# Optimization experiments

Measured on AMD Instinct MI355X. Metric: run time of the kernel, lower is better.

The kernel has to match this reference:

```python
import jax, jax.numpy as jnp
import numpy as np

N, M, P = 128, 16, 256   # speakers, utterances/speaker, projection dim
W, B = 10.0, -5.0        # GE2E scale/bias (abs(w)*s + b)
EPS_NORM = 1e-12
EPS_LOG = 1e-9


def setup_inputs() -> dict:
    key = jax.random.key(0)
    e = jax.random.normal(key, (N * M, P), dtype=jnp.float32)
    return {"e": e}


def _l2norm(x):
    return x / jnp.sqrt(jnp.sum(x * x, axis=-1, keepdims=True) + EPS_NORM)


def _similarity(e):
    # i_eq_j: [N*M, N], row k has 1 in column k//M
    eye = jnp.repeat(jnp.eye(N, dtype=e.dtype), M, axis=0)
    i = eye[:, :, None]                               # [N*M, N, 1]
    spk = e.reshape(N, M, P)
    cent_sum = jnp.sum(spk, axis=1)                   # [N, P] full centroid sums
    # leave-one-out subtraction only where i==j: [N*M, N, P]
    centroids = cent_sum[None, :, :] - i * e[:, None, :]
    # scale: /(m-1) for own speaker (leave-one-out), /m otherwise
    centroids = (i / (M - 1) + (1.0 - i) / M) * centroids
    e_n = _l2norm(e)                                  # [N*M, P]
    c_n = _l2norm(centroids)                          # [N*M, N, P]
    s = jnp.einsum('kp,knp->kn', e_n, c_n)            # [N*M, N]
    return s


def reference(e):
    eye = jnp.repeat(jnp.eye(N, dtype=e.dtype), M, axis=0)
    s = jnp.abs(W) * _similarity(e) + B               # [N*M, N]
    s_jij = jnp.sum(s * eye, axis=-1)                 # [N*M]
    softmax = jnp.log(jnp.sum(jnp.exp(s), axis=-1) + EPS_LOG)
    loss = jnp.mean(-s_jij + softmax)
    return (loss, s)
```

## Files before the change

kernel.cpp:

```cpp
#include <hip/hip_runtime.h>
#include <math.h>

#define N_CL 128
#define M_SPK 16
#define P_DIM 256
#define NM 2048
static constexpr float EPS_NORM = 1e-12f;
static constexpr float EPS_LOG  = 1e-9f;
static constexpr float W_ABS    = 10.0f;
static constexpr float B_OFF    = -5.0f;

#define WS_CENTT   0
#define WS_CSN     32768
#define WS_SCALE   32896
#define WS_ENORM2  33024
#define WS_RE      35072
#define WS_ROWLOSS 37120

__device__ __forceinline__ float waveReduceSum(float x) {
    #pragma unroll
    for (int off = 32; off > 0; off >>= 1)
        x += __shfl_xor(x, off, 64);
    return x;
}

__global__ __launch_bounds__(256)
void k1_stats(const float* __restrict__ e, float* __restrict__ ws) {
    const int n    = blockIdx.x;
    const int p    = threadIdx.x;
    const int wid  = p >> 6;
    const int lane = p & 63;

    float* centT     = ws + WS_CENTT;
    float* csn       = ws + WS_CSN;
    float* scale_oth = ws + WS_SCALE;
    float* enorm2    = ws + WS_ENORM2;
    float* re        = ws + WS_RE;

    __shared__ float part[M_SPK][4];
    __shared__ float cpart[4];

    float acc = 0.f;
    #pragma unroll
    for (int m = 0; m < M_SPK; ++m) {
        float v = e[(n * M_SPK + m) * P_DIM + p];
        acc += v;
        float sq = waveReduceSum(v * v);
        if (lane == 0) part[m][wid] = sq;
    }
    centT[p * N_CL + n] = acc;

    float c2 = waveReduceSum(acc * acc);
    if (lane == 0) cpart[wid] = c2;
    __syncthreads();

    if (p < M_SPK) {
        int row = n * M_SPK + p;
        float s2 = part[p][0] + part[p][1] + part[p][2] + part[p][3];
        enorm2[row] = s2;
        re[row] = 1.0f / sqrtf(s2 + EPS_NORM);
    }
    if (p == 0) {
        float t = cpart[0] + cpart[1] + cpart[2] + cpart[3];
        csn[n] = t;
        scale_oth[n] = 1.0f / sqrtf(t + (float)(M_SPK * M_SPK) * EPS_NORM);
    }
}

__global__ __launch_bounds__(128)
void k2_main(const float* __restrict__ e, const float* __restrict__ ws,
             float* __restrict__ d_out, float* __restrict__ rowloss) {
    const int k = blockIdx.x;
    const int t = threadIdx.x;

    const float* centT     = ws + WS_CENTT;
    const float* csn       = ws + WS_CSN;
    const float* scale_oth = ws + WS_SCALE;
    const float* enorm2    = ws + WS_ENORM2;
    const float* re        = ws + WS_RE;

    __shared__ float eL[P_DIM];
    __shared__ float wpart[2];
    __shared__ float sOwn;

    eL[t]       = e[k * P_DIM + t];
    eL[t + 128] = e[k * P_DIM + 128 + t];
    __syncthreads();

    float dot = 0.f;
    #pragma unroll 16
    for (int p = 0; p < P_DIM; ++p)
        dot = fmaf(eL[p], centT[p * N_CL + t], dot);

    const int nk = k >> 4;
    const float rek = re[k];
    float s;
    if (t == nk) {
        const float e2  = enorm2[k];
        const float num = (dot - e2) * (1.0f / (M_SPK - 1));
        const float h2  = (csn[nk] - 2.0f * dot + e2)
                          * (1.0f / ((M_SPK - 1) * (M_SPK - 1)));
        s = W_ABS * (num * rek / sqrtf(h2 + EPS_NORM)) + B_OFF;
        sOwn = s;
    } else {
        s = W_ABS * (dot * rek * scale_oth[t]) + B_OFF;
    }
    d_out[1 + k * N_CL + t] = s;

    float ex = expf(s);
    float wsum = waveReduceSum(ex);
    const int lane = t & 63;
    const int wid  = t >> 6;
    if (lane == 0) wpart[wid] = wsum;
    __syncthreads();
    if (t == 0) {
        float tot = wpart[0] + wpart[1];
        rowloss[k] = logf(tot + EPS_LOG) - sOwn;
    }
}

__global__ __launch_bounds__(256)
void k3_reduce(const float* __restrict__ rowloss, float* __restrict__ d_out) {
    __shared__ float wpart[4];
    const int t = threadIdx.x;
    float sum = 0.f;
    #pragma unroll
    for (int i = 0; i < NM / 256; ++i)
        sum += rowloss[i * 256 + t];
    sum = waveReduceSum(sum);
    if ((t & 63) == 0) wpart[t >> 6] = sum;
    __syncthreads();
    if (t == 0)
        d_out[0] = (wpart[0] + wpart[1] + wpart[2] + wpart[3]) * (1.0f / NM);
}

extern "C" void kernel_launch(void* const* d_in, const int* in_sizes, int n_in,
                              void* d_out, int out_size, void* d_ws, size_t ws_size,
                              hipStream_t stream) {
    const float* e = (const float*)d_in[0];
    float* out = (float*)d_out;
    float* ws  = (float*)d_ws;

    k1_stats<<<N_CL, 256, 0, stream>>>(e, ws);
    k2_main<<<NM, 128, 0, stream>>>(e, ws, out, ws + WS_ROWLOSS);
    k3_reduce<<<1, 256, 0, stream>>>(ws + WS_ROWLOSS, out);
}
```

Baseline: 23.99 us.

## Fuse similarity and loss reduction into one kernel with last-block atomic reduce

Removes the third reduction kernel by having the last finishing block of the main kernel sum per-block losses, detected through an atomic counter. Each block now handles 8 rows instead of one, so every centroid load is reused across 4 rows per wave. Row and centroid norms are recomputed inside the main kernel instead of being precomputed in a stats kernel, which slims the first kernel. This trades a launch and some redundant norm work for more register pressure and an atomic-ordering dependency.

```diff
diff --git a/kernel.cpp b/kernel.cpp
--- a/kernel.cpp
+++ b/kernel.cpp
@@ -5,17 +5,13 @@
 #define M_SPK 16
 #define P_DIM 256
 #define NM 2048
+#define NBLK 256
 static constexpr float EPS_NORM = 1e-12f;
 static constexpr float EPS_LOG  = 1e-9f;
-static constexpr float W_ABS    = 10.0f;
-static constexpr float B_OFF    = -5.0f;
 
-#define WS_CENTT   0
-#define WS_CSN     32768
-#define WS_SCALE   32896
-#define WS_ENORM2  33024
-#define WS_RE      35072
-#define WS_ROWLOSS 37120
+#define WS_CENTT     0
+#define WS_BLOCKLOSS 32768
+#define WS_CNT       33024
 
 __device__ __forceinline__ float waveReduceSum(float x) {
     #pragma unroll
@@ -25,113 +21,130 @@
 }
 
 __global__ __launch_bounds__(256)
-void k1_stats(const float* __restrict__ e, float* __restrict__ ws) {
-    const int n    = blockIdx.x;
-    const int p    = threadIdx.x;
-    const int wid  = p >> 6;
-    const int lane = p & 63;
-
-    float* centT     = ws + WS_CENTT;
-    float* csn       = ws + WS_CSN;
-    float* scale_oth = ws + WS_SCALE;
-    float* enorm2    = ws + WS_ENORM2;
-    float* re        = ws + WS_RE;
-
-    __shared__ float part[M_SPK][4];
-    __shared__ float cpart[4];
-
+void k1_cent(const float* __restrict__ e, float* __restrict__ ws,
+             unsigned* __restrict__ cnt) {
+    const int n = blockIdx.x;
+    const int p = threadIdx.x;
+    const float* base = e + (size_t)n * (M_SPK * P_DIM) + p;
     float acc = 0.f;
     #pragma unroll
-    for (int m = 0; m < M_SPK; ++m) {
-        float v = e[(n * M_SPK + m) * P_DIM + p];
-        acc += v;
-        float sq = waveReduceSum(v * v);
-        if (lane == 0) part[m][wid] = sq;
-    }
-    centT[p * N_CL + n] = acc;
-
-    float c2 = waveReduceSum(acc * acc);
-    if (lane == 0) cpart[wid] = c2;
-    __syncthreads();
-
-    if (p < M_SPK) {
-        int row = n * M_SPK + p;
-        float s2 = part[p][0] + part[p][1] + part[p][2] + part[p][3];
-        enorm2[row] = s2;
-        re[row] = 1.0f / sqrtf(s2 + EPS_NORM);
-    }
-    if (p == 0) {
-        float t = cpart[0] + cpart[1] + cpart[2] + cpart[3];
-        csn[n] = t;
-        scale_oth[n] = 1.0f / sqrtf(t + (float)(M_SPK * M_SPK) * EPS_NORM);
-    }
-}
-
-__global__ __launch_bounds__(128)
-void k2_main(const float* __restrict__ e, const float* __restrict__ ws,
-             float* __restrict__ d_out, float* __restrict__ rowloss) {
-    const int k = blockIdx.x;
-    const int t = threadIdx.x;
-
-    const float* centT     = ws + WS_CENTT;
-    const float* csn       = ws + WS_CSN;
-    const float* scale_oth = ws + WS_SCALE;
-    const float* enorm2    = ws + WS_ENORM2;
-    const float* re        = ws + WS_RE;
-
-    __shared__ float eL[P_DIM];
-    __shared__ float wpart[2];
-    __shared__ float sOwn;
-
-    eL[t]       = e[k * P_DIM + t];
-    eL[t + 128] = e[k * P_DIM + 128 + t];
-    __syncthreads();
-
-    float dot = 0.f;
-    #pragma unroll 16
-    for (int p = 0; p < P_DIM; ++p)
-        dot = fmaf(eL[p], centT[p * N_CL + t], dot);
-
-    const int nk = k >> 4;
-    const float rek = re[k];
-    float s;
-    if (t == nk) {
-        const float e2  = enorm2[k];
-        const float num = (dot - e2) * (1.0f / (M_SPK - 1));
-        const float h2  = (csn[nk] - 2.0f * dot + e2)
-                          * (1.0f / ((M_SPK - 1) * (M_SPK - 1)));
-        s = W_ABS * (num * rek / sqrtf(h2 + EPS_NORM)) + B_OFF;
-        sOwn = s;
-    } else {
-        s = W_ABS * (dot * rek * scale_oth[t]) + B_OFF;
-    }
-    d_out[1 + k * N_CL + t] = s;
-
-    float ex = expf(s);
-    float wsum = waveReduceSum(ex);
-    const int lane = t & 63;
-    const int wid  = t >> 6;
-    if (lane == 0) wpart[wid] = wsum;
-    __syncthreads();
-    if (t == 0) {
-        float tot = wpart[0] + wpart[1];
-        rowloss[k] = logf(tot + EPS_LOG) - sOwn;
-    }
+    for (int m = 0; m < M_SPK; ++m) acc += base[m * P_DIM];
+    ws[WS_CENTT + p * N_CL + n] = acc;
+    if (n == 0 && p == 0) *cnt = 0u;
 }
 
 __global__ __launch_bounds__(256)
-void k3_reduce(const float* __restrict__ rowloss, float* __restrict__ d_out) {
-    __shared__ float wpart[4];
-    const int t = threadIdx.x;
-    float sum = 0.f;
+void k2_fused(const float* __restrict__ e, const float* __restrict__ ws_ro,
+              float* __restrict__ d_out, float* __restrict__ blockloss,
+              unsigned* __restrict__ cnt) {
+    const int bid  = blockIdx.x;
+    const int t    = threadIdx.x;
+    const int lane = t & 63;
+    const int w    = t >> 6;
+    const int g    = w & 1;
+    const int h    = w >> 1;
+    const int k0   = bid * 8;
+    const int nk   = k0 >> 4;
+    const int np   = h * 64 + lane;
+
+    const float* centT = ws_ro + WS_CENTT;
+
+    __shared__ float eL[8][P_DIM];
+    __shared__ float partial[8][2];
+    __shared__ float own_s[8];
+    __shared__ float vv[8];
+    __shared__ float wp[4];
+    __shared__ int   lastFlag;
+
     #pragma unroll
-    for (int i = 0; i < NM / 256; ++i)
-        sum += rowloss[i * 256 + t];
-    sum = waveReduceSum(sum);
-    if ((t & 63) == 0) wpart[t >> 6] = sum;
+    for (int i = 0; i < 8; ++i)
+        ((float*)eL)[i * 256 + t] = e[(size_t)k0 * P_DIM + i * 256 + t];
+    if (t == 0) lastFlag = 0;
     __syncthreads();
-    if (t == 0)
-        d_out[0] = (wpart[0] + wpart[1] + wpart[2] + wpart[3]) * (1.0f / NM);
+
+    float e2[4], rek[4];
+    #pragma unroll
+    for (int r = 0; r < 4; ++r) {
+        const float* row = eL[4 * g + r];
+        float x0 = row[lane], x1 = row[lane + 64], x2 = row[lane + 128], x3 = row[lane + 192];
+        float s2 = waveReduceSum(x0 * x0 + x1 * x1 + x2 * x2 + x3 * x3);
+        e2[r]  = s2;
+        rek[r] = 1.0f / sqrtf(s2 + EPS_NORM);
+    }
+
+    float dot[4] = {0.f, 0.f, 0.f, 0.f};
+    float cacc = 0.f;
+    const float* cptr = centT + np;
+    #pragma unroll 2
+    for (int p = 0; p < P_DIM; p += 4) {
+        float c0 = cptr[(p + 0) * N_CL];
+        float c1 = cptr[(p + 1) * N_CL];
+        float c2 = cptr[(p + 2) * N_CL];
+        float c3 = cptr[(p + 3) * N_CL];
+        cacc = fmaf(c0, c0, cacc);
+        cacc = fmaf(c1, c1, cacc);
+        cacc = fmaf(c2, c2, cacc);
+        cacc = fmaf(c3, c3, cacc);
+        #pragma unroll
+        for (int r = 0; r < 4; ++r) {
+            float4 ev = *(const float4*)&eL[4 * g + r][p];
+            dot[r] = fmaf(ev.x, c0, dot[r]);
+            dot[r] = fmaf(ev.y, c1, dot[r]);
+            dot[r] = fmaf(ev.z, c2, dot[r]);
+            dot[r] = fmaf(ev.w, c3, dot[r]);
+        }
+    }
+
+    const float sc_oth = 1.0f / sqrtf(cacc + (float)(M_SPK * M_SPK) * EPS_NORM);
+    float svals[4];
+    #pragma unroll
+    for (int r = 0; r < 4; ++r) {
+        float s;
+        if (np == nk) {
+            float num = (dot[r] - e2[r]) * (1.0f / 15.0f);
+            float hh  = (cacc - 2.0f * dot[r] + e2[r]) * (1.0f / 225.0f);
+            s = 10.0f * (num * rek[r] / sqrtf(hh + EPS_NORM)) - 5.0f;
+        } else {
+            s = 10.0f * (dot[r] * rek[r] * sc_oth) - 5.0f;
+        }
+        svals[r] = s;
+        const int k = k0 + 4 * g + r;
+        d_out[1 + (size_t)k * N_CL + np] = s;
+    }
+    #pragma unroll
+    for (int r = 0; r < 4; ++r) {
+        float exsum = waveReduceSum(expf(svals[r]));
+        if (lane == 0) partial[4 * g + r][h] = exsum;
+    }
+    if (np == nk) {
+        #pragma unroll
+        for (int r = 0; r < 4; ++r) own_s[4 * g + r] = svals[r];
+    }
+    __syncthreads();
+
+    if (t < 8) {
+        float tot = partial[t][0] + partial[t][1];
+        vv[t] = logf(tot + EPS_LOG) - own_s[t];
+    }
+    __syncthreads();
+
+    if (t == 0) {
+        float bl = 0.f;
+        #pragma unroll
+        for (int i = 0; i < 8; ++i) bl += vv[i];
+        __hip_atomic_store(&blockloss[bid], bl, __ATOMIC_RELAXED, __HIP_MEMORY_SCOPE_AGENT);
+        unsigned old = __hip_atomic_fetch_add(cnt, 1u, __ATOMIC_ACQ_REL, __HIP_MEMORY_SCOPE_AGENT);
+        lastFlag = (old == NBLK - 1) ? 1 : 0;
+    }
+    __syncthreads();
+
+    if (lastFlag) {
+        float v = __hip_atomic_load(&blockloss[t], __ATOMIC_RELAXED, __HIP_MEMORY_SCOPE_AGENT);
+        float sum = waveReduceSum(v);
+        if (lane == 0) wp[w] = sum;
+        __syncthreads();
+        if (t == 0) d_out[0] = (wp[0] + wp[1] + wp[2] + wp[3]) * (1.0f / NM);
+    }
 }
 
 extern "C" void kernel_launch(void* const* d_in, const int* in_sizes, int n_in,
@@ -140,8 +153,8 @@
     const float* e = (const float*)d_in[0];
     float* out = (float*)d_out;
     float* ws  = (float*)d_ws;
+    unsigned* cnt = (unsigned*)(ws + WS_CNT);
 
-    k1_stats<<<N_CL, 256, 0, stream>>>(e, ws);
-    k2_main<<<NM, 128, 0, stream>>>(e, ws, out, ws + WS_ROWLOSS);
-    k3_reduce<<<1, 256, 0, stream>>>(ws + WS_ROWLOSS, out);
+    k1_cent<<<N_CL, 256, 0, stream>>>(e, ws, cnt);
+    k2_fused<<<NBLK, 256, 0, stream>>>(e, ws, out, ws + WS_BLOCKLOSS, cnt);
 }
```

New measurement: 28.54 us. +19.0%, slower.
